# Kernel tuning notes

Measured on AMD Instinct MI355X. Metric: run time of the kernel, lower is better.

Reference implementation:

```python
import jax, jax.numpy as jnp
import numpy as np
from jax import lax

B, S, D = 8, 96, 768
R, RSEQ, TAG = 24, 8, 3


def setup_inputs() -> dict:
    key = jax.random.key(0)
    k0, k1, k2, k3 = jax.random.split(key, 4)
    encoded_text = jax.random.normal(k0, (B, S, D), jnp.float32)
    rel_types_encoded = jax.random.normal(k1, (R, RSEQ, D), jnp.float32)
    proj_W = jax.random.normal(k2, (2 * D, 3 * D), jnp.float32) * 0.02
    proj_b = jnp.zeros((3 * D,), jnp.float32)
    rel_W = jax.random.normal(k3, (3 * D, R * TAG), jnp.float32) * 0.02
    rel_b = jnp.zeros((R * TAG,), jnp.float32)
    return {
        "encoded_text": encoded_text,
        "rel_types_encoded": rel_types_encoded,
        "proj_W": proj_W,
        "proj_b": proj_b,
        "rel_W": rel_W,
        "rel_b": rel_b,
    }


def _refine(enc, rel_types):
    """Faithful vectorized version of the nested python loops in
    get_encoded_text: for each sample i, R sequential cross-attention
    updates on matrix_b using matrix_a = rel_types_encoded[i] (the
    original code indexes with i, reusing the same matrix_a each step).
    enc: [Bsz, S, D]; rel_types: [R, RSEQ, D].
    """
    Bsz = enc.shape[0]
    d = enc.shape[-1]
    scale = 1.0 / jnp.sqrt(jnp.asarray(d, enc.dtype))
    num_steps = rel_types.shape[0]  # loop runs rel_types_encoded.size(0) times
    A_batch = rel_types[:Bsz]  # matrix_a = rel_types_encoded[i]

    def per_sample(b0, A):  # b0: [S, D], A: [RSEQ, D]
        def step(b, _):
            scores = (A @ b.T) * scale            # [RSEQ, S]
            w = jax.nn.softmax(scores, axis=-1)    # softmax over seq
            return b + w.T @ A, None               # matrix_b += matrix_c
        bf, _ = lax.scan(step, b0, None, length=num_steps)
        return bf

    return jax.vmap(per_sample)(enc, A_batch)


def reference(encoded_text, rel_types_encoded, proj_W, proj_b, rel_W, rel_b):
    enc = _refine(encoded_text, rel_types_encoded)  # [B, S, D]
    Bsz, seq, d = enc.shape
    rel_num = rel_types_encoded.shape[0]
    tag_size = rel_W.shape[1] // rel_num

    # projection(cat(head, tail)) == head @ Wh + tail @ Wt + b; avoid
    # materializing the [B, S*S, 2D] concat (same math as the original).
    Wh, Wt = proj_W[:d], proj_W[d:]
    Hh = enc @ Wh                                   # [B, S, 3D] head part
    Ht = enc @ Wt                                   # [B, S, 3D] tail part
    pairs = Hh[:, :, None, :] + Ht[:, None, :, :] + proj_b  # [B, S, S, 3D]
    pairs = jax.nn.relu(pairs)
    triple = pairs.reshape(Bsz, seq * seq, 3 * d) @ rel_W + rel_b
    triple = triple.reshape(Bsz, seq, seq, rel_num, tag_size)
    return jnp.transpose(triple, (0, 4, 3, 1, 2))  # [B, tag, rel, S, S]
```

## Files before the change

kernel.cpp:

```cpp
#include <hip/hip_runtime.h>
#include <hip/hip_bf16.h>
#include <math.h>
#include <stdint.h>
#include <string.h>

#define BB 8
#define SS 96
#define DD 768
#define RR 24
#define RSEQ 8
#define TAG 3
#define D3 2304
#define NC 72

typedef __attribute__((ext_vector_type(8))) short bf16x8;
typedef __attribute__((ext_vector_type(4))) float f32x4;
typedef _Float16 f16x8 __attribute__((ext_vector_type(8)));
typedef _Float16 f16x2 __attribute__((ext_vector_type(2)));

typedef __attribute__((address_space(3))) uint8_t lds_u8;
typedef const __attribute__((address_space(1))) uint8_t glb_u8;
static __device__ __forceinline__ void glld16(const void* g, void* l) {
  __builtin_amdgcn_global_load_lds((glb_u8*)g, (lds_u8*)l, 16, 0, 0);
}

#define VMW(N) asm volatile("s_waitcnt vmcnt(" #N ")" ::: "memory")

static __device__ inline uint32_t pkrhu(float lo, float hi) {
  uint32_t a, b;
  memcpy(&a, &lo, 4);
  memcpy(&b, &hi, 4);
  return __builtin_amdgcn_perm(b + 0x8000u, a + 0x8000u, 0x07060302u);
}
static __device__ inline uint32_t pkrne(float lo, float hi) {
  uint32_t a, b;
  memcpy(&a, &lo, 4);
  memcpy(&b, &hi, 4);
  a += 0x7FFFu + ((a >> 16) & 1u);
  b += 0x7FFFu + ((b >> 16) & 1u);
  return (a >> 16) | (b & 0xFFFF0000u);
}
static __device__ inline uint32_t pkf16(float lo, float hi) {
  union { f16x2 h; uint32_t u; } r;
  r.h[0] = (_Float16)lo;
  r.h[1] = (_Float16)hi;
  return r.u;
}
static __device__ inline uint16_t f16b(float v) {
  union { _Float16 h; uint16_t u; } r;
  r.h = (_Float16)v;
  return r.u;
}

__global__ __launch_bounds__(256) void k_prep0(const float* __restrict__ relW,
                                               uint16_t* __restrict__ Wb,
                                               const float* __restrict__ projW,
                                               uint16_t* __restrict__ Tp,
                                               const float* __restrict__ enc,
                                               const float* __restrict__ rel,
                                               float* __restrict__ SG) {
  __shared__ __align__(16) char smem[24704];
  const int blk = blockIdx.x;
  const int t = threadIdx.x;

  if (blk < 36) {
    float* tile = (float*)smem;
    const int k0 = blk * 64;
    const float* src = relW + (size_t)k0 * NC;
    for (int e = t; e < 64 * NC / 4; e += 256) ((float4*)tile)[e] = ((const float4*)src)[e];
    __syncthreads();
    for (int u = t; u < 80 * 16; u += 256) {
      const int n = u >> 4, kq = (u & 15) * 4;
      uint2 w = {0u, 0u};
      if (n < NC) {
        w.x = pkf16(tile[(kq + 0) * NC + n], tile[(kq + 1) * NC + n]);
        w.y = pkf16(tile[(kq + 2) * NC + n], tile[(kq + 3) * NC + n]);
      }
      *(uint2*)&Wb[(size_t)n * D3 + k0 + kq] = w;
    }
  } else if (blk < 900) {
    const int bx = blk - 36;
    float (*tile)[65] = (float(*)[65])smem;
    const int c0 = (bx % 36) * 64;
    const int r0 = (bx / 36) * 64;
    {
      const int tr = t >> 4;
      const int tc4 = (t & 15) * 4;
#pragma unroll
      for (int p = 0; p < 4; ++p) {
        const int r = tr + p * 16;
        const float4 v = *(const float4*)&projW[(size_t)(r0 + r) * D3 + c0 + tc4];
        tile[r][tc4 + 0] = v.x;
        tile[r][tc4 + 1] = v.y;
        tile[r][tc4 + 2] = v.z;
        tile[r][tc4 + 3] = v.w;
      }
    }
    __syncthreads();
    {
      const int cc = t >> 4;
      const int rr4 = (t & 15) * 4;
#pragma unroll
      for (int p = 0; p < 4; ++p) {
        const int c = cc + p * 16;
        uint2 w;
        w.x = pkrne(tile[rr4 + 0][c], tile[rr4 + 1][c]);
        w.y = pkrne(tile[rr4 + 2][c], tile[rr4 + 3][c]);
        *(uint2*)&Tp[(size_t)(c0 + c) * (2 * DD) + r0 + rr4] = w;
      }
    }
  } else {
    const int idx = blk - 900;
    const int b = idx >> 4;
    const int d0 = (idx & 15) * 48;
    float (*AsF)[48] = (float(*)[48])smem;

    if (t < 96) {
      const int r = t / 12, q4 = (t % 12) * 4;
      *(float4*)&AsF[r][q4] = *(const float4*)&rel[((size_t)b * RSEQ + r) * DD + d0 + q4];
    }
    __syncthreads();

    for (int e = t; e < RSEQ * (SS + RSEQ); e += 256) {
      const int r = e & 7, s = e >> 3;
      const float* row = (s < SS) ? (enc + ((size_t)b * SS + s) * DD + d0) : &AsF[s - SS][0];
      float a0 = 0.f, a1 = 0.f, a2 = 0.f, a3 = 0.f;
#pragma unroll
      for (int d = 0; d < 48; d += 4) {
        const float4 rv = *(const float4*)&row[d];
        a0 += AsF[r][d + 0] * rv.x;
        a1 += AsF[r][d + 1] * rv.y;
        a2 += AsF[r][d + 2] * rv.z;
        a3 += AsF[r][d + 3] * rv.w;
      }
      atomicAdd(&SG[((size_t)b * RSEQ + r) * 104 + s], (a0 + a1) + (a2 + a3));
    }
  }
}

__global__ __launch_bounds__(256) void k_refS(const float* __restrict__ SG,
                                              float* __restrict__ Pst) {
  const int b = blockIdx.x;
  const int t = threadIdx.x;
  __shared__ float S0[RSEQ][SS];
  __shared__ float G[RSEQ][RSEQ];
  __shared__ float P[RSEQ][SS];
  __shared__ float sc[RSEQ][SS];
  const float scale = 0.036084391824351613f;

  for (int e = t; e < RSEQ * 104; e += 256) {
    const int r = e / 104, c = e % 104;
    const float v = SG[(size_t)b * RSEQ * 104 + e];
    if (c < SS) S0[r][c] = v;
    else G[r][c - SS] = v;
  }
  for (int e = t; e < RSEQ * SS; e += 256) ((float*)P)[e] = 0.f;
  __syncthreads();

  const int wave = t >> 6, lane = t & 63;
  for (int step = 0; step < RR; ++step) {
    for (int e = t; e < RSEQ * SS; e += 256) {
      const int r = e / SS, s = e % SS;
      float acc = S0[r][s];
#pragma unroll
      for (int r2 = 0; r2 < RSEQ; ++r2) acc += G[r][r2] * P[r2][s];
      sc[r][s] = acc * scale;
    }
    __syncthreads();
#pragma unroll
    for (int rr = 0; rr < 2; ++rr) {
      const int r = wave * 2 + rr;
      const float m1 = sc[r][lane];
      const float m2 = (lane < 32) ? sc[r][lane + 64] : -1e30f;
      float mx = fmaxf(m1, m2);
#pragma unroll
      for (int o = 32; o > 0; o >>= 1) mx = fmaxf(mx, __shfl_xor(mx, o, 64));
      const float e1 = __expf(m1 - mx);
      const float e2 = (lane < 32) ? __expf(m2 - mx) : 0.f;
      float sm = e1 + e2;
#pragma unroll
      for (int o = 32; o > 0; o >>= 1) sm += __shfl_xor(sm, o, 64);
      const float inv = 1.f / sm;
      P[r][lane] += e1 * inv;
      if (lane < 32) P[r][lane + 64] += e2 * inv;
    }
    __syncthreads();
  }

  for (int e = t; e < RSEQ * SS; e += 256) Pst[(size_t)b * RSEQ * SS + e] = ((float*)P)[e];
}

__global__ __launch_bounds__(256) void k_refB(const float* __restrict__ enc,
                                              const float* __restrict__ rel,
                                              const float* __restrict__ Pst,
                                              uint16_t* __restrict__ encRb) {
  const int blk = blockIdx.x;
  const int b = blk / 12;
  const int s0 = (blk % 12) * 8;
  const int t = threadIdx.x;
  __shared__ float As[RSEQ][DD + 4];
  __shared__ float Pl[RSEQ][8];

  const float* Ag = rel + (size_t)b * RSEQ * DD;
  for (int e = t; e < RSEQ * DD / 4; e += 256) {
    const int r = (e * 4) / DD, d = (e * 4) % DD;
    *(float4*)&As[r][d] = *(const float4*)&Ag[e * 4];
  }
  if (t < RSEQ * 8) {
    const int r = t >> 3, sl = t & 7;
    Pl[r][sl] = Pst[(size_t)b * RSEQ * SS + r * SS + s0 + sl];
  }
  __syncthreads();

  const float* Eb = enc + ((size_t)b * SS + s0) * DD;
  uint16_t* Ob = encRb + ((size_t)b * SS + s0) * DD;
  for (int e = t; e < 8 * DD / 4; e += 256) {
    const int sl = (e * 4) / DD, d = (e * 4) % DD;
    float4 v = ((const float4*)Eb)[e];
#pragma unroll
    for (int r = 0; r < RSEQ; ++r) {
      const float p = Pl[r][sl];
      v.x += p * As[r][d + 0];
      v.y += p * As[r][d + 1];
      v.z += p * As[r][d + 2];
      v.w += p * As[r][d + 3];
    }
    uint2 w;
    w.x = pkrhu(v.x, v.y);
    w.y = pkrhu(v.z, v.w);
    *(uint2*)&Ob[e * 4] = w;
  }
}

__global__ __launch_bounds__(256, 4) void k_proj(const uint16_t* __restrict__ Ab,
                                                 const uint16_t* __restrict__ Bt,
                                                 const float* __restrict__ pb,
                                                 uint16_t* __restrict__ Hh16,
                                                 uint16_t* __restrict__ Htf) {
  const int m0 = blockIdx.x * 128;
  const int gn0 = blockIdx.y * 64;
  const bool isH = gn0 < D3;
  const int n0 = isH ? gn0 : gn0 - D3;
  const int halfk = isH ? 0 : DD;
  const int t = threadIdx.x, w = t >> 6, lane = t & 63;
  const int wm = w >> 1, wn = w & 1;
  const int lm = lane & 15, q = lane >> 4;

  __shared__ __align__(16) uint16_t As[128 * 72];
  __shared__ __align__(16) uint16_t Bs[64 * 72];

  const char* rp[7];
  char* lp[7];
#pragma unroll
  for (int r = 0; r < 7; ++r) {
    const int idx = w + 4 * r;
    rp[r] = nullptr;
    lp[r] = nullptr;
    if (idx < 27) {
      const int ii = (idx < 18) ? idx : idx - 18;
      const int beta = ii * 1024 + lane * 16;
      const int elem = beta >> 1;
      const int row = elem / 72;
      int o = elem - row * 72;
      if (o >= 64) o = 0;
      if (idx < 18) {
        rp[r] = (const char*)(Ab + (size_t)(m0 + row) * DD + o);
        lp[r] = (char*)As + ii * 1024;
      } else {
        rp[r] = (const char*)(Bt + (size_t)(n0 + row) * (2 * DD) + halfk + o);
        lp[r] = (char*)Bs + ii * 1024;
      }
    }
  }

  f32x4 acc[4][2];
#pragma unroll
  for (int a = 0; a < 4; ++a)
#pragma unroll
    for (int c = 0; c < 2; ++c) acc[a][c] = (f32x4){0.f, 0.f, 0.f, 0.f};

  for (int k0 = 0; k0 < DD; k0 += 64) {
    __syncthreads();
#pragma unroll
    for (int r = 0; r < 7; ++r)
      if (rp[r]) glld16(rp[r] + 2 * k0, lp[r]);
    __syncthreads();
#pragma unroll
    for (int kk = 0; kk < 2; ++kk) {
      const int ko = kk * 32 + q * 8;
      bf16x8 af[4], bf[2];
#pragma unroll
      for (int mt = 0; mt < 4; ++mt)
        af[mt] = *(const bf16x8*)&As[(wm * 64 + mt * 16 + lm) * 72 + ko];
#pragma unroll
      for (int nt = 0; nt < 2; ++nt)
        bf[nt] = *(const bf16x8*)&Bs[(wn * 32 + nt * 16 + lm) * 72 + ko];
#pragma unroll
      for (int nt = 0; nt < 2; ++nt)
#pragma unroll
        for (int mt = 0; mt < 4; ++mt)
          acc[mt][nt] = __builtin_amdgcn_mfma_f32_16x16x32_bf16(af[mt], bf[nt], acc[mt][nt], 0, 0, 0);
    }
  }

#pragma unroll
  for (int nt = 0; nt < 2; ++nt) {
    const int ncol = n0 + wn * 32 + nt * 16 + lm;
    const int mrow = m0 + wm * 64 + q * 4;
    uint16_t* dst = isH ? Hh16 : Htf;
    const float bias = isH ? pb[ncol] : 0.f;
#pragma unroll
    for (int mt = 0; mt < 4; ++mt)
#pragma unroll
      for (int r = 0; r < 4; ++r)
        dst[(size_t)(mrow + mt * 16 + r) * D3 + ncol] = f16b(acc[mt][nt][r] + bias);
  }
}

#define HT_LDS 12288
#define CH_B 22528
#define NISS 22
#define NKC 36
#define NPH 18

__global__ __launch_bounds__(768, 1) void k_pairs(const uint16_t* __restrict__ Hh,
                                                  const uint16_t* __restrict__ Htb,
                                                  const uint16_t* __restrict__ Wb,
                                                  const float* __restrict__ relb,
                                                  float* __restrict__ out) {
  const int blk = blockIdx.x;
  const int b = blk >> 5, ii = blk & 31;
  const int t = threadIdx.x;
  const int w = t >> 6, lane = t & 63;
  const int lm = lane & 15, q = lane >> 4;
  const int iw = w >> 2;
  const int jh = (w >> 1) & 1;
  const int kh = w & 1;
  const int i = ii * 3 + iw;

  __shared__ __align__(16) uint16_t Hr[7680];
  __shared__ __align__(16) uint16_t Stg[3][CH_B];

  {
    const char* hh = (const char*)(Hh + ((size_t)b * SS + ii * 3) * D3);
#pragma unroll
    for (int r = 0; r < 2; ++r) {
      const int idx = w + 12 * r;
      if (idx < 14) glld16(hh + idx * 1024 + lane * 16, (char*)Hr + idx * 1024);
    }
  }

  const char* rp[2];
#pragma unroll
  for (int r = 0; r < 2; ++r) {
    const int idx = w + 12 * r;
    rp[r] = nullptr;
    if (idx < NISS) {
      const int beta = idx * 1024 + lane * 16;
      if (beta < HT_LDS) {
        const int row = beta >> 7;
        const int real = (beta & 127) ^ ((row & 7) << 4);
        rp[r] = (const char*)(Htb + ((size_t)b * SS + row) * D3 + (real >> 1));
      } else {
        const int bb = beta - HT_LDS;
        const int row = bb >> 7;
        const int real = (bb & 127) ^ ((row & 7) << 4);
        rp[r] = (const char*)(Wb + (size_t)row * D3 + (real >> 1));
      }
    }
  }

#pragma unroll
  for (int pp = 0; pp < 2; ++pp)
#pragma unroll
    for (int kc = 0; kc < 2; ++kc)
#pragma unroll
      for (int r = 0; r < 2; ++r)
        if (rp[r])
          glld16(rp[r] + (size_t)128 * (2 * pp + kc),
                 (char*)Stg[pp] + kc * CH_B + (w + 12 * r) * 1024);

  f32x4 acc[3][5];
#pragma unroll
  for (int mt = 0; mt < 3; ++mt)
#pragma unroll
    for (int nt = 0; nt < 5; ++nt) acc[mt][nt] = (f32x4){0.f, 0.f, 0.f, 0.f};

  const f16x8 zro = {0, 0, 0, 0, 0, 0, 0, 0};

  for (int p = 0; p < NPH; ++p) {
    if (w < 10) VMW(4); else VMW(2);
    __builtin_amdgcn_s_barrier();
    __builtin_amdgcn_sched_barrier(0);

    {
      char* dst = (char*)Stg[(p + 2) % 3];
      int pn = p + 2;
      if (pn >= NPH) pn -= NPH;
#pragma unroll
      for (int kc = 0; kc < 2; ++kc)
#pragma unroll
        for (int r = 0; r < 2; ++r)
          if (rp[r])
            glld16(rp[r] + (size_t)128 * (2 * pn + kc),
                   dst + kc * CH_B + (w + 12 * r) * 1024);
    }

    const char* S = (const char*)Stg[p % 3] + kh * CH_B;
    const int k0 = (2 * p + kh) * 64;
#pragma unroll
    for (int kk = 0; kk < 2; ++kk) {
      const int ko = kk * 32 + q * 8;
      const int xb = (ko * 2) ^ ((lane & 7) << 4);
      const f16x8 hv = *(const f16x8*)&Hr[iw * D3 + k0 + ko];
      f16x8 af[3];
#pragma unroll
      for (int mt = 0; mt < 3; ++mt) {
        const f16x8 s = *(const f16x8*)(S + (jh * 48 + mt * 16 + lm) * 128 + xb) + hv;
        af[mt] = __builtin_elementwise_max(s, zro);
      }
      f16x8 bfv[5];
#pragma unroll
      for (int nt = 0; nt < 5; ++nt)
        bfv[nt] = *(const f16x8*)(S + HT_LDS + (nt * 16 + lm) * 128 + xb);
      __builtin_amdgcn_s_setprio(1);
#pragma unroll
      for (int nt = 0; nt < 5; ++nt)
#pragma unroll
        for (int mt = 0; mt < 3; ++mt)
          acc[mt][nt] = __builtin_amdgcn_mfma_f32_16x16x32_f16(af[mt], bfv[nt], acc[mt][nt], 0, 0, 0);
      __builtin_amdgcn_s_setprio(0);
    }
    asm volatile("s_waitcnt lgkmcnt(0)" ::: "memory");
    __builtin_amdgcn_sched_barrier(0);
  }

  __syncthreads();
  float* RED = (float*)&Stg[0][0];
  if (w & 1) {
#pragma unroll
    for (int mt = 0; mt < 3; ++mt)
#pragma unroll
      for (int nt = 0; nt < 5; ++nt)
        *(f32x4*)&RED[(((w >> 1) * 15 + mt * 5 + nt) << 8) + lane * 4] = acc[mt][nt];
  }
  __syncthreads();
  if (!(w & 1)) {
#pragma unroll
    for (int nt = 0; nt < 5; ++nt) {
      const int c = nt * 16 + lm;
      if (c < NC) {
        const float rb = relb[c];
        const int rr = c / 3, tg = c % 3;
#pragma unroll
        for (int mt = 0; mt < 3; ++mt) {
          const f32x4 oth = *(const f32x4*)&RED[(((w >> 1) * 15 + mt * 5 + nt) << 8) + lane * 4];
          const int j0 = jh * 48 + mt * 16 + q * 4;
          float* base = out + ((((size_t)b * TAG + tg) * RR + rr) * SS + i) * SS + j0;
          float4 o;
          o.x = acc[mt][nt][0] + oth[0] + rb;
          o.y = acc[mt][nt][1] + oth[1] + rb;
          o.z = acc[mt][nt][2] + oth[2] + rb;
          o.w = acc[mt][nt][3] + oth[3] + rb;
          *(float4*)base = o;
        }
      }
    }
  }
}

extern "C" void kernel_launch(void* const* d_in, const int* in_sizes, int n_in,
                              void* d_out, int out_size, void* d_ws, size_t ws_size,
                              hipStream_t stream) {
  const float* enc   = (const float*)d_in[0];
  const float* rel   = (const float*)d_in[1];
  const float* projW = (const float*)d_in[2];
  const float* projb = (const float*)d_in[3];
  const float* relW  = (const float*)d_in[4];
  const float* relb  = (const float*)d_in[5];
  float* out = (float*)d_out;

  uint16_t* Hh16 = (uint16_t*)d_ws;
  uint16_t* Htf  = Hh16 + (size_t)DD * D3 + 512;
  uint16_t* Wb   = Htf + (size_t)DD * D3;
  uint16_t* Tp   = Wb + (size_t)96 * D3;
  uint16_t* Ab   = Tp + (size_t)D3 * 2 * DD;
  float* Pst = (float*)(Ab + (size_t)DD * DD);
  float* SG = Pst + (size_t)BB * RSEQ * SS;

  hipMemsetAsync(SG, 0, (size_t)BB * RSEQ * 104 * sizeof(float), stream);
  k_prep0<<<1028, 256, 0, stream>>>(relW, Wb, projW, Tp, enc, rel, SG);
  k_refS<<<BB, 256, 0, stream>>>(SG, Pst);
  k_refB<<<96, 256, 0, stream>>>(enc, rel, Pst, Ab);
  k_proj<<<dim3(6, 72), 256, 0, stream>>>(Ab, Tp, projb, Hh16, Htf);
  k_pairs<<<256, 768, 0, stream>>>(Hh16, Htf, Wb, relb, out);
}
```

Baseline: 181.5 us.

## Overlap serial refinement with weight conversion by regrouping prep kernels

The S/G score computation moves into its own small kernel. The serial 24-step softmax refinement is fused with the encoder update into 8 blocks of a new kernel. That kernel's other blocks do the relW and projW bf16/f16 conversion. The long serial refinement chain now runs alongside the weight-conversion work, and one launch plus the Pst round-trip through global memory go away. In exchange, the encoder-update work sits on only 8 blocks, and the larger shared memory may lower occupancy for the transpose blocks.

New measurement: 205.2 us. 13.0% more time.

```diff
diff --git a/kernel.cpp b/kernel.cpp
--- a/kernel.cpp
+++ b/kernel.cpp
@@ -52,20 +52,125 @@
   return r.u;
 }
 
-__global__ __launch_bounds__(256) void k_prep0(const float* __restrict__ relW,
-                                               uint16_t* __restrict__ Wb,
-                                               const float* __restrict__ projW,
-                                               uint16_t* __restrict__ Tp,
-                                               const float* __restrict__ enc,
-                                               const float* __restrict__ rel,
-                                               float* __restrict__ SG) {
-  __shared__ __align__(16) char smem[24704];
+__global__ __launch_bounds__(256) void k_prepSG(const float* __restrict__ enc,
+                                                const float* __restrict__ rel,
+                                                float* __restrict__ SG) {
+  __shared__ __align__(16) float AsF[RSEQ][48];
+  const int idx = blockIdx.x;
+  const int t = threadIdx.x;
+  const int b = idx >> 4;
+  const int d0 = (idx & 15) * 48;
+
+  if (t < 96) {
+    const int r = t / 12, q4 = (t % 12) * 4;
+    *(float4*)&AsF[r][q4] = *(const float4*)&rel[((size_t)b * RSEQ + r) * DD + d0 + q4];
+  }
+  __syncthreads();
+
+  for (int e = t; e < RSEQ * (SS + RSEQ); e += 256) {
+    const int r = e & 7, s = e >> 3;
+    const float* row = (s < SS) ? (enc + ((size_t)b * SS + s) * DD + d0) : &AsF[s - SS][0];
+    float a0 = 0.f, a1 = 0.f, a2 = 0.f, a3 = 0.f;
+#pragma unroll
+    for (int d = 0; d < 48; d += 4) {
+      const float4 rv = *(const float4*)&row[d];
+      a0 += AsF[r][d + 0] * rv.x;
+      a1 += AsF[r][d + 1] * rv.y;
+      a2 += AsF[r][d + 2] * rv.z;
+      a3 += AsF[r][d + 3] * rv.w;
+    }
+    atomicAdd(&SG[((size_t)b * RSEQ + r) * 104 + s], (a0 + a1) + (a2 + a3));
+  }
+}
+
+__global__ __launch_bounds__(256) void k_refR(const float* __restrict__ SG,
+                                              const float* __restrict__ enc,
+                                              const float* __restrict__ rel,
+                                              const float* __restrict__ relW,
+                                              uint16_t* __restrict__ Wb,
+                                              const float* __restrict__ projW,
+                                              uint16_t* __restrict__ Tp,
+                                              uint16_t* __restrict__ encRb) {
+  __shared__ __align__(16) char smem[34176];
   const int blk = blockIdx.x;
   const int t = threadIdx.x;
 
-  if (blk < 36) {
+  if (blk < 8) {
+    const int b = blk;
+    float (*S0)[SS] = (float(*)[SS])smem;
+    float (*G)[RSEQ] = (float(*)[RSEQ])(smem + 3072);
+    float (*P)[SS] = (float(*)[SS])(smem + 3328);
+    float (*sc)[SS] = (float(*)[SS])(smem + 6400);
+    float (*As)[DD + 4] = (float(*)[DD + 4])(smem + 9472);
+    const float scale = 0.036084391824351613f;
+
+    for (int e = t; e < RSEQ * 104; e += 256) {
+      const int r = e / 104, c = e % 104;
+      const float v = SG[(size_t)b * RSEQ * 104 + e];
+      if (c < SS) S0[r][c] = v;
+      else G[r][c - SS] = v;
+    }
+    for (int e = t; e < RSEQ * SS; e += 256) ((float*)P)[e] = 0.f;
+    __syncthreads();
+
+    const int wave = t >> 6, lane = t & 63;
+    for (int step = 0; step < RR; ++step) {
+      for (int e = t; e < RSEQ * SS; e += 256) {
+        const int r = e / SS, s = e % SS;
+        float acc = S0[r][s];
+#pragma unroll
+        for (int r2 = 0; r2 < RSEQ; ++r2) acc += G[r][r2] * P[r2][s];
+        sc[r][s] = acc * scale;
+      }
+      __syncthreads();
+#pragma unroll
+      for (int rr = 0; rr < 2; ++rr) {
+        const int r = wave * 2 + rr;
+        const float m1 = sc[r][lane];
+        const float m2 = (lane < 32) ? sc[r][lane + 64] : -1e30f;
+        float mx = fmaxf(m1, m2);
+#pragma unroll
+        for (int o = 32; o > 0; o >>= 1) mx = fmaxf(mx, __shfl_xor(mx, o, 64));
+        const float e1 = __expf(m1 - mx);
+        const float e2 = (lane < 32) ? __expf(m2 - mx) : 0.f;
+        float sm = e1 + e2;
+#pragma unroll
+        for (int o = 32; o > 0; o >>= 1) sm += __shfl_xor(sm, o, 64);
+        const float inv = 1.f / sm;
+        P[r][lane] += e1 * inv;
+        if (lane < 32) P[r][lane + 64] += e2 * inv;
+      }
+      __syncthreads();
+    }
+
+    const float* Ag = rel + (size_t)b * RSEQ * DD;
+    for (int e = t; e < RSEQ * DD / 4; e += 256) {
+      const int r = (e * 4) / DD, d = (e * 4) % DD;
+      *(float4*)&As[r][d] = *(const float4*)&Ag[e * 4];
+    }
+    __syncthreads();
+
+    const float* Eb = enc + (size_t)b * SS * DD;
+    uint16_t* Ob = encRb + (size_t)b * SS * DD;
+    for (int e = t; e < SS * DD / 4; e += 256) {
+      const int s = (e * 4) / DD, d = (e * 4) % DD;
+      float4 v = ((const float4*)Eb)[e];
+#pragma unroll
+      for (int r = 0; r < RSEQ; ++r) {
+        const float p = P[r][s];
+        v.x += p * As[r][d + 0];
+        v.y += p * As[r][d + 1];
+        v.z += p * As[r][d + 2];
+        v.w += p * As[r][d + 3];
+      }
+      uint2 w;
+      w.x = pkrhu(v.x, v.y);
+      w.y = pkrhu(v.z, v.w);
+      *(uint2*)&Ob[e * 4] = w;
+    }
+  } else if (blk < 44) {
     float* tile = (float*)smem;
-    const int k0 = blk * 64;
+    const int k0 = (blk - 8) * 64;
     const float* src = relW + (size_t)k0 * NC;
     for (int e = t; e < 64 * NC / 4; e += 256) ((float4*)tile)[e] = ((const float4*)src)[e];
     __syncthreads();
@@ -78,8 +183,8 @@
       }
       *(uint2*)&Wb[(size_t)n * D3 + k0 + kq] = w;
     }
-  } else if (blk < 900) {
-    const int bx = blk - 36;
+  } else {
+    const int bx = blk - 44;
     float (*tile)[65] = (float(*)[65])smem;
     const int c0 = (bx % 36) * 64;
     const int r0 = (bx / 36) * 64;
@@ -109,126 +214,6 @@
         *(uint2*)&Tp[(size_t)(c0 + c) * (2 * DD) + r0 + rr4] = w;
       }
     }
-  } else {
-    const int idx = blk - 900;
-    const int b = idx >> 4;
-    const int d0 = (idx & 15) * 48;
-    float (*AsF)[48] = (float(*)[48])smem;
-
-    if (t < 96) {
-      const int r = t / 12, q4 = (t % 12) * 4;
-      *(float4*)&AsF[r][q4] = *(const float4*)&rel[((size_t)b * RSEQ + r) * DD + d0 + q4];
-    }
-    __syncthreads();
-
-    for (int e = t; e < RSEQ * (SS + RSEQ); e += 256) {
-      const int r = e & 7, s = e >> 3;
-      const float* row = (s < SS) ? (enc + ((size_t)b * SS + s) * DD + d0) : &AsF[s - SS][0];
-      float a0 = 0.f, a1 = 0.f, a2 = 0.f, a3 = 0.f;
-#pragma unroll
-      for (int d = 0; d < 48; d += 4) {
-        const float4 rv = *(const float4*)&row[d];
-        a0 += AsF[r][d + 0] * rv.x;
-        a1 += AsF[r][d + 1] * rv.y;
-        a2 += AsF[r][d + 2] * rv.z;
-        a3 += AsF[r][d + 3] * rv.w;
-      }
-      atomicAdd(&SG[((size_t)b * RSEQ + r) * 104 + s], (a0 + a1) + (a2 + a3));
-    }
-  }
-}
-
-__global__ __launch_bounds__(256) void k_refS(const float* __restrict__ SG,
-                                              float* __restrict__ Pst) {
-  const int b = blockIdx.x;
-  const int t = threadIdx.x;
-  __shared__ float S0[RSEQ][SS];
-  __shared__ float G[RSEQ][RSEQ];
-  __shared__ float P[RSEQ][SS];
-  __shared__ float sc[RSEQ][SS];
-  const float scale = 0.036084391824351613f;
-
-  for (int e = t; e < RSEQ * 104; e += 256) {
-    const int r = e / 104, c = e % 104;
-    const float v = SG[(size_t)b * RSEQ * 104 + e];
-    if (c < SS) S0[r][c] = v;
-    else G[r][c - SS] = v;
-  }
-  for (int e = t; e < RSEQ * SS; e += 256) ((float*)P)[e] = 0.f;
-  __syncthreads();
-
-  const int wave = t >> 6, lane = t & 63;
-  for (int step = 0; step < RR; ++step) {
-    for (int e = t; e < RSEQ * SS; e += 256) {
-      const int r = e / SS, s = e % SS;
-      float acc = S0[r][s];
-#pragma unroll
-      for (int r2 = 0; r2 < RSEQ; ++r2) acc += G[r][r2] * P[r2][s];
-      sc[r][s] = acc * scale;
-    }
-    __syncthreads();
-#pragma unroll
-    for (int rr = 0; rr < 2; ++rr) {
-      const int r = wave * 2 + rr;
-      const float m1 = sc[r][lane];
-      const float m2 = (lane < 32) ? sc[r][lane + 64] : -1e30f;
-      float mx = fmaxf(m1, m2);
-#pragma unroll
-      for (int o = 32; o > 0; o >>= 1) mx = fmaxf(mx, __shfl_xor(mx, o, 64));
-      const float e1 = __expf(m1 - mx);
-      const float e2 = (lane < 32) ? __expf(m2 - mx) : 0.f;
-      float sm = e1 + e2;
-#pragma unroll
-      for (int o = 32; o > 0; o >>= 1) sm += __shfl_xor(sm, o, 64);
-      const float inv = 1.f / sm;
-      P[r][lane] += e1 * inv;
-      if (lane < 32) P[r][lane + 64] += e2 * inv;
-    }
-    __syncthreads();
-  }
-
-  for (int e = t; e < RSEQ * SS; e += 256) Pst[(size_t)b * RSEQ * SS + e] = ((float*)P)[e];
-}
-
-__global__ __launch_bounds__(256) void k_refB(const float* __restrict__ enc,
-                                              const float* __restrict__ rel,
-                                              const float* __restrict__ Pst,
-                                              uint16_t* __restrict__ encRb) {
-  const int blk = blockIdx.x;
-  const int b = blk / 12;
-  const int s0 = (blk % 12) * 8;
-  const int t = threadIdx.x;
-  __shared__ float As[RSEQ][DD + 4];
-  __shared__ float Pl[RSEQ][8];
-
-  const float* Ag = rel + (size_t)b * RSEQ * DD;
-  for (int e = t; e < RSEQ * DD / 4; e += 256) {
-    const int r = (e * 4) / DD, d = (e * 4) % DD;
-    *(float4*)&As[r][d] = *(const float4*)&Ag[e * 4];
-  }
-  if (t < RSEQ * 8) {
-    const int r = t >> 3, sl = t & 7;
-    Pl[r][sl] = Pst[(size_t)b * RSEQ * SS + r * SS + s0 + sl];
-  }
-  __syncthreads();
-
-  const float* Eb = enc + ((size_t)b * SS + s0) * DD;
-  uint16_t* Ob = encRb + ((size_t)b * SS + s0) * DD;
-  for (int e = t; e < 8 * DD / 4; e += 256) {
-    const int sl = (e * 4) / DD, d = (e * 4) % DD;
-    float4 v = ((const float4*)Eb)[e];
-#pragma unroll
-    for (int r = 0; r < RSEQ; ++r) {
-      const float p = Pl[r][sl];
-      v.x += p * As[r][d + 0];
-      v.y += p * As[r][d + 1];
-      v.z += p * As[r][d + 2];
-      v.w += p * As[r][d + 3];
-    }
-    uint2 w;
-    w.x = pkrhu(v.x, v.y);
-    w.y = pkrhu(v.z, v.w);
-    *(uint2*)&Ob[e * 4] = w;
   }
 }
 
@@ -489,9 +474,8 @@
   float* SG = Pst + (size_t)BB * RSEQ * SS;
 
   hipMemsetAsync(SG, 0, (size_t)BB * RSEQ * 104 * sizeof(float), stream);
-  k_prep0<<<1028, 256, 0, stream>>>(relW, Wb, projW, Tp, enc, rel, SG);
-  k_refS<<<BB, 256, 0, stream>>>(SG, Pst);
-  k_refB<<<96, 256, 0, stream>>>(enc, rel, Pst, Ab);
+  k_prepSG<<<128, 256, 0, stream>>>(enc, rel, SG);
+  k_refR<<<908, 256, 0, stream>>>(SG, enc, rel, relW, Wb, projW, Tp, Ab);
   k_proj<<<dim3(6, 72), 256, 0, stream>>>(Ab, Tp, projb, Hh16, Htf);
   k_pairs<<<256, 768, 0, stream>>>(Hh16, Htf, Wb, relb, out);
 }
```
